# Optimization experiments

Hardware: AMD Instinct MI355X
Metric: run time of the kernel (lower is better)

The kernel has to match this reference:

```python
import jax, jax.numpy as jnp
import numpy as np

B, N, D, E = 4, 8192, 8, 128
SCALE = float(1.0 / np.sqrt(E))  # torch MHA scaling, n_heads=1 -> head_dim=E


def _attn_dir(X, idx, mask, Wq, Wk, Wv, ipw, ipb, ow, ob):
    # X: [B,N,E]; idx, mask: [B,N,D]. Sequence per node = [self] + padded neighbors.
    neigh = jax.vmap(lambda x, i: x[i])(X, idx)               # [B,N,D,E] gather
    seq = jnp.concatenate([X[:, :, None, :], neigh], axis=2)  # [B,N,1+D,E]
    m = jnp.concatenate([jnp.ones(mask.shape[:2] + (1,), bool), mask.astype(bool)], axis=2)
    wq, wk, wv = jnp.split(ipw, 3, axis=0)                    # torch in_proj_weight [3E,E]
    bq, bk, bv = jnp.split(ipb, 3)
    # custom pre-projections (X @ W), then torch MHA in_proj (x @ w.T + b)
    q = (X @ Wq) @ wq.T + bq                                  # [B,N,E]; only self row queried
    k = (seq @ Wk) @ wk.T + bk                                # [B,N,1+D,E]
    v = (seq @ Wv) @ wv.T + bv                                # [B,N,1+D,E]
    scores = jnp.einsum('bne,bnse->bns', q, k) * SCALE
    scores = jnp.where(m, scores, jnp.finfo(scores.dtype).min)
    w = jax.nn.softmax(scores, axis=-1)
    ctx = jnp.einsum('bns,bnse->bne', w, v)
    return ctx @ ow.T + ob                                    # MHA out_proj


def setup_inputs():
    key = jax.random.key(0)
    ks = jax.random.split(key, 26)
    f32 = jnp.float32
    inp = {
        "X": jax.random.normal(ks[0], (B, N, E), f32),
        "in_idx": jax.random.randint(ks[1], (B, N, D), 0, N, dtype=jnp.int32),
        "out_idx": jax.random.randint(ks[2], (B, N, D), 0, N, dtype=jnp.int32),
        "in_mask": jax.random.randint(ks[3], (B, N, D), 0, 2, dtype=jnp.int32),
        "out_mask": jax.random.randint(ks[4], (B, N, D), 0, 2, dtype=jnp.int32),
    }
    i = 5
    for pfx in ("in_", "out_"):
        inp[pfx + "Wq"] = jax.random.uniform(ks[i], (E, E), f32) * 0.1; i += 1
        inp[pfx + "Wk"] = jax.random.uniform(ks[i], (E, E), f32) * 0.1; i += 1
        inp[pfx + "Wv"] = jax.random.uniform(ks[i], (E, E), f32) * 0.1; i += 1
        inp[pfx + "ipw"] = jax.random.normal(ks[i], (3 * E, E), f32) * 0.05; i += 1
        inp[pfx + "ipb"] = jax.random.normal(ks[i], (3 * E,), f32) * 0.02; i += 1
        inp[pfx + "ow"] = jax.random.normal(ks[i], (E, E), f32) * 0.05; i += 1
        inp[pfx + "ob"] = jax.random.normal(ks[i], (E,), f32) * 0.02; i += 1
    inp["lin_w"] = jax.random.normal(ks[i], (E, 2 * E), f32) * 0.05; i += 1
    inp["lin_b"] = jax.random.normal(ks[i], (E,), f32) * 0.02
    return inp


def reference(X, in_idx, out_idx, in_mask, out_mask,
              in_Wq, in_Wk, in_Wv, in_ipw, in_ipb, in_ow, in_ob,
              out_Wq, out_Wk, out_Wv, out_ipw, out_ipb, out_ow, out_ob,
              lin_w, lin_b):
    a_in = _attn_dir(X, in_idx, in_mask, in_Wq, in_Wk, in_Wv, in_ipw, in_ipb, in_ow, in_ob)
    a_out = _attn_dir(X, out_idx, out_mask, out_Wq, out_Wk, out_Wv, out_ipw, out_ipb, out_ow, out_ob)
    h = jnp.concatenate([a_in, a_out], axis=-1) @ lin_w.T + lin_b  # [B,N,E]
    return jax.nn.elu(h)
```

## Files before the change

### kernel.cpp

```cpp
#include <hip/hip_runtime.h>
#include <math.h>

#define NNODE 32768
constexpr float SCALE = 0.08838834764831845f;

typedef unsigned short u16;
typedef __bf16 bf16x8 __attribute__((ext_vector_type(8)));
typedef float f32x4 __attribute__((ext_vector_type(4)));

__device__ __forceinline__ u16 f2bf(float f) {
    unsigned u = __float_as_uint(f);
    u += 0x7fff + ((u >> 16) & 1);
    return (u16)(u >> 16);
}
__device__ __forceinline__ unsigned pack2bf(float lo, float hi) {
    return (unsigned)f2bf(lo) | ((unsigned)f2bf(hi) << 16);
}
__device__ __forceinline__ void unpack8(uint4 u, float* f) {
    f[0] = __uint_as_float(u.x << 16);  f[1] = __uint_as_float(u.x & 0xffff0000u);
    f[2] = __uint_as_float(u.y << 16);  f[3] = __uint_as_float(u.y & 0xffff0000u);
    f[4] = __uint_as_float(u.z << 16);  f[5] = __uint_as_float(u.z & 0xffff0000u);
    f[6] = __uint_as_float(u.w << 16);  f[7] = __uint_as_float(u.w & 0xffff0000u);
}
__device__ __forceinline__ float dot128(const float* __restrict__ a,
                                        const float* __restrict__ b) {
    float s = 0.f;
    #pragma unroll
    for (int c = 0; c < 128; c += 4) {
        float4 x = *(const float4*)&a[c];
        float4 y = *(const float4*)&b[c];
        s = fmaf(x.x, y.x, s); s = fmaf(x.y, y.y, s);
        s = fmaf(x.z, y.z, s); s = fmaf(x.w, y.w, s);
    }
    return s;
}

__device__ __forceinline__ void gl_lds16(const void* g, void* l) {
    __builtin_amdgcn_global_load_lds(
        (const __attribute__((address_space(1))) unsigned int*)(uintptr_t)g,
        (__attribute__((address_space(3))) unsigned int*)(unsigned int)(uintptr_t)l,
        16, 0, 0);
}

__global__ __launch_bounds__(256) void wprep1(
    const float* __restrict__ ipw_in, const float* __restrict__ ipw_out,
    const float* __restrict__ Wq_in, const float* __restrict__ Wk_in,
    const float* __restrict__ Wv_in,
    const float* __restrict__ Wq_out, const float* __restrict__ Wk_out,
    const float* __restrict__ Wv_out,
    const float* __restrict__ ow_in, const float* __restrict__ ow_out,
    const float* __restrict__ lin_w,
    float* __restrict__ Af, float* __restrict__ Bmf,
    float* __restrict__ Wtf, float* __restrict__ RTf)
{
    int t = blockIdx.x * 256 + threadIdx.x;
    int i = t >> 7, j = t & 127;
    int task = blockIdx.y, dir = task & 1, kind = task >> 1;
    if (kind < 3) {
        const float* ipw = dir ? ipw_out : ipw_in;
        const float* W; const float* w; float* outp;
        if (kind == 0)      { W = dir ? Wq_out : Wq_in; w = ipw;          outp = Af;  }
        else if (kind == 1) { W = dir ? Wk_out : Wk_in; w = ipw + 16384;  outp = Bmf; }
        else                { W = dir ? Wv_out : Wv_in; w = ipw + 32768;  outp = Wtf; }
        outp[dir * 16384 + i * 128 + j] = dot128(W + i * 128, w + j * 128);
    } else {
        const float* ow = dir ? ow_out : ow_in;
        const float* lw = lin_w + i * 256 + dir * 128;
        float s = 0.f;
        #pragma unroll
        for (int e = 0; e < 128; e += 4) {
            float4 l4 = *(const float4*)&lw[e];
            s = fmaf(ow[e * 128 + j],       l4.x, s);
            s = fmaf(ow[(e + 1) * 128 + j], l4.y, s);
            s = fmaf(ow[(e + 2) * 128 + j], l4.z, s);
            s = fmaf(ow[(e + 3) * 128 + j], l4.w, s);
        }
        RTf[dir * 16384 + i * 128 + j] = s;
    }
}

__global__ __launch_bounds__(256) void wprep2(
    const float* __restrict__ Af, const float* __restrict__ Bmf,
    const float* __restrict__ Wtf, const float* __restrict__ RTf,
    const float* __restrict__ ipb_in, const float* __restrict__ ipb_out,
    const float* __restrict__ lin_w, const float* __restrict__ lin_b,
    const float* __restrict__ ob_in, const float* __restrict__ ob_out,
    u16* __restrict__ Bcat, u16* __restrict__ QfT,
    float* __restrict__ ycat, float* __restrict__ bfin)
{
    int task = blockIdx.y;
    int t = blockIdx.x * 256 + threadIdx.x;
    if (task < 2) {
        int dir = task, i = t >> 7, j = t & 127;
        float s = dot128(Af + dir * 16384 + j * 128, Bmf + dir * 16384 + i * 128);
        Bcat[(size_t)(dir * 128 + i) * 128 + j] = f2bf(s);
    } else if (task < 4) {
        int dir = task - 2, i = t >> 7, j = t & 127;
        float s = dot128(Wtf + dir * 16384 + j * 128, RTf + dir * 16384 + i * 128);
        QfT[(size_t)i * 256 + dir * 128 + j] = f2bf(s);
    } else {
        if (t < 256) {
            int dir = t >> 7, d = t & 127;
            const float* bq = dir ? ipb_out : ipb_in;
            const float* rb = Bmf + dir * 16384 + d * 128;
            float s = 0.f;
            for (int f = 0; f < 128; ++f) s = fmaf(rb[f], bq[f], s);
            ycat[t] = s;
        } else if (t < 384) {
            int g = t - 256;
            float s = lin_b[g];
            #pragma unroll
            for (int dir = 0; dir < 2; ++dir) {
                const float* bv = (dir ? ipb_out : ipb_in) + 256;
                const float* rt = RTf + dir * 16384 + g * 128;
                const float* ob = dir ? ob_out : ob_in;
                const float* lw = lin_w + g * 256 + dir * 128;
                for (int c = 0; c < 128; ++c)
                    s += bv[c] * rt[c] + ob[c] * lw[c];
            }
            bfin[g] = s;
        }
    }
}

template<int NT>
__global__ __launch_bounds__(256) void gemm_y(
    const float* __restrict__ X,
    const u16* __restrict__ BT,
    const float* __restrict__ bias,
    u16* __restrict__ C, u16* __restrict__ Xb)
{
    __shared__ __align__(16) u16 As[128 * 128];
    __shared__ __align__(16) u16 Bs[128 * 128];
    const int tid  = threadIdx.x;
    const int lane = tid & 63;
    const int wid  = tid >> 6;
    const int bm  = blockIdx.x * 128;
    const int wr = wid >> 1, wc = wid & 1;
    const int l15 = lane & 15, l4 = lane >> 4;

    #pragma unroll
    for (int i = 0; i < 8; ++i) {
        int c = i * 256 + tid;
        int r = c >> 4, cb = c & 15;
        const float* src = &X[(size_t)(bm + r) * 128 + cb * 8];
        float4 f0 = *(const float4*)src;
        float4 f1 = *(const float4*)(src + 4);
        uint4 pk;
        pk.x = pack2bf(f0.x, f0.y); pk.y = pack2bf(f0.z, f0.w);
        pk.z = pack2bf(f1.x, f1.y); pk.w = pack2bf(f1.z, f1.w);
        *(uint4*)&As[r * 128 + ((cb ^ (r & 7)) * 8)] = pk;
        *(uint4*)&Xb[(size_t)(bm + r) * 128 + cb * 8] = pk;
    }
    __syncthreads();
    bf16x8 a[4][4];
    #pragma unroll
    for (int ks = 0; ks < 4; ++ks)
        #pragma unroll
        for (int mr = 0; mr < 4; ++mr) {
            int r = wr * 64 + mr * 16 + l15;
            int kb = ks * 4 + l4;
            a[ks][mr] = *(const bf16x8*)((const char*)As + r * 256 + ((kb ^ (r & 7)) << 4));
        }

    #pragma unroll
    for (int nt = 0; nt < NT; ++nt) {
        int bn = nt * 128;
        __syncthreads();
        #pragma unroll
        for (int i = 0; i < 8; ++i) {
            int c = i * 256 + tid;
            int r = c >> 4, cb = c & 15;
            gl_lds16(&BT[(size_t)(bn + r) * 128 + 8 * (cb ^ (r & 7))],
                     &Bs[(size_t)(c - lane) * 8]);
        }
        __syncthreads();

        f32x4 acc[4][4] = {};
        #pragma unroll
        for (int ks = 0; ks < 4; ++ks) {
            bf16x8 bfr[4];
            #pragma unroll
            for (int nc = 0; nc < 4; ++nc) {
                int r = wc * 64 + nc * 16 + l15;
                int kb = ks * 4 + l4;
                bfr[nc] = *(const bf16x8*)((const char*)Bs + r * 256 + ((kb ^ (r & 7)) << 4));
            }
            #pragma unroll
            for (int mr = 0; mr < 4; ++mr)
                #pragma unroll
                for (int nc = 0; nc < 4; ++nc)
                    acc[mr][nc] = __builtin_amdgcn_mfma_f32_16x16x32_bf16(
                        a[ks][mr], bfr[nc], acc[mr][nc], 0, 0, 0);
        }
        #pragma unroll
        for (int nc = 0; nc < 4; ++nc) {
            int col = bn + wc * 64 + nc * 16 + l15;
            float bv = bias[col];
            #pragma unroll
            for (int mr = 0; mr < 4; ++mr)
                #pragma unroll
                for (int j = 0; j < 4; ++j) {
                    int row = bm + wr * 64 + mr * 16 + l4 * 4 + j;
                    C[(size_t)row * 256 + col] = f2bf(acc[mr][nc][j] + bv);
                }
        }
    }
}

template<int KTOT, bool ELU_F32>
__global__ __launch_bounds__(256) void gemm_mfma(
    const u16* __restrict__ A,
    const u16* __restrict__ BT,
    const float* __restrict__ bias,
    void* __restrict__ Cout, int ldc)
{
    __shared__ __align__(16) u16 As[128 * 128];
    __shared__ __align__(16) u16 Bs[128 * 128];
    const int tid  = threadIdx.x;
    const int lane = tid & 63;
    const int wid  = tid >> 6;
    const int bm = blockIdx.x * 128;
    const int bn = blockIdx.y * 128;
    const int wr = wid >> 1, wc = wid & 1;
    const int l15 = lane & 15, l4 = lane >> 4;

    f32x4 acc[4][4] = {};

    for (int k0 = 0; k0 < KTOT; k0 += 128) {
        #pragma unroll
        for (int i = 0; i < 8; ++i) {
            int c = i * 256 + tid;
            int r = c >> 4, cb = c & 15;
            int col = k0 + 8 * (cb ^ (r & 7));
            gl_lds16(&A[(size_t)(bm + r) * KTOT + col], &As[(size_t)(c - lane) * 8]);
            gl_lds16(&BT[(size_t)(bn + r) * KTOT + col], &Bs[(size_t)(c - lane) * 8]);
        }
        __syncthreads();
        #pragma unroll
        for (int ks = 0; ks < 4; ++ks) {
            bf16x8 a[4], b[4];
            #pragma unroll
            for (int mr = 0; mr < 4; ++mr) {
                int r = wr * 64 + mr * 16 + l15;
                int kb = ks * 4 + l4;
                a[mr] = *(const bf16x8*)((const char*)As + r * 256 + ((kb ^ (r & 7)) << 4));
            }
            #pragma unroll
            for (int nc = 0; nc < 4; ++nc) {
                int r = wc * 64 + nc * 16 + l15;
                int kb = ks * 4 + l4;
                b[nc] = *(const bf16x8*)((const char*)Bs + r * 256 + ((kb ^ (r & 7)) << 4));
            }
            #pragma unroll
            for (int mr = 0; mr < 4; ++mr)
                #pragma unroll
                for (int nc = 0; nc < 4; ++nc)
                    acc[mr][nc] = __builtin_amdgcn_mfma_f32_16x16x32_bf16(
                        a[mr], b[nc], acc[mr][nc], 0, 0, 0);
        }
        __syncthreads();
    }

    #pragma unroll
    for (int nc = 0; nc < 4; ++nc) {
        int col = bn + wc * 64 + nc * 16 + l15;
        float bv = bias[col];
        #pragma unroll
        for (int mr = 0; mr < 4; ++mr) {
            #pragma unroll
            for (int j = 0; j < 4; ++j) {
                int row = bm + wr * 64 + mr * 16 + l4 * 4 + j;
                float v = acc[mr][nc][j] + bv;
                if (ELU_F32) {
                    v = v > 0.f ? v : (__expf(v) - 1.f);
                    ((float*)Cout)[(size_t)row * ldc + col] = v;
                } else {
                    ((u16*)Cout)[(size_t)row * ldc + col] = f2bf(v);
                }
            }
        }
    }
}

__global__ __launch_bounds__(256) void attn_kernel(
    const u16* __restrict__ Y, const u16* __restrict__ Xb,
    const int* __restrict__ in_idx, const int* __restrict__ out_idx,
    const int* __restrict__ in_mask, const int* __restrict__ out_mask,
    u16* __restrict__ XCTX)
{
    const int tid = threadIdx.x;
    const int g   = tid >> 4;
    const int l   = tid & 15;
    const int pair = blockIdx.x & 7;
    const int dir = pair & 1, b = pair >> 1;
    const int nl = ((blockIdx.x >> 3) << 4) + g;
    const int node = (b << 13) + nl;
    const int* idx = dir == 0 ? in_idx : out_idx;
    const int* msk = dir == 0 ? in_mask : out_mask;

    const int4 i0 = *(const int4*)&idx[(size_t)node * 8];
    const int4 i1 = *(const int4*)&idx[(size_t)node * 8 + 4];
    const int4 m0 = *(const int4*)&msk[(size_t)node * 8];
    const int4 m1 = *(const int4*)&msk[(size_t)node * 8 + 4];
    const int ii[8] = { i0.x, i0.y, i0.z, i0.w, i1.x, i1.y, i1.z, i1.w };
    const int mm[8] = { m0.x, m0.y, m0.z, m0.w, m1.x, m1.y, m1.z, m1.w };

    uint4 yv = *(const uint4*)&Y[(size_t)node * 256 + dir * 128 + l * 8];
    uint4 xv[9];
    xv[0] = *(const uint4*)&Xb[(size_t)node * 128 + l * 8];
    #pragma unroll
    for (int s = 0; s < 8; ++s)
        xv[s + 1] = *(const uint4*)&Xb[(size_t)((b << 13) + ii[s]) * 128 + l * 8];

    float yf[8];
    unpack8(yv, yf);
    float sc[9];
    #pragma unroll
    for (int s = 0; s < 9; ++s) {
        float kf[8];
        unpack8(xv[s], kf);
        float d = 0.f;
        #pragma unroll
        for (int j = 0; j < 8; ++j) d = fmaf(yf[j], kf[j], d);
        sc[s] = d;
    }

    #pragma unroll
    for (int s = 0; s < 9; ++s) {
        float x = sc[s];
        x += __shfl_xor(x, 1);
        x += __shfl_xor(x, 2);
        x += __shfl_xor(x, 4);
        x += __shfl_xor(x, 8);
        sc[s] = x * SCALE;
    }
    #pragma unroll
    for (int s = 1; s < 9; ++s)
        sc[s] = mm[s - 1] ? sc[s] : -1e30f;

    float m = sc[0];
    #pragma unroll
    for (int s = 1; s < 9; ++s) m = fmaxf(m, sc[s]);
    float w[9], wsum = 0.f;
    #pragma unroll
    for (int s = 0; s < 9; ++s) { w[s] = __expf(sc[s] - m); wsum += w[s]; }
    const float inv = 1.f / wsum;

    float acc[8] = {};
    #pragma unroll
    for (int s = 0; s < 9; ++s) {
        float vf[8];
        unpack8(xv[s], vf);
        #pragma unroll
        for (int j = 0; j < 8; ++j) acc[j] = fmaf(w[s], vf[j], acc[j]);
    }
    uint4 o;
    o.x = pack2bf(acc[0] * inv, acc[1] * inv);
    o.y = pack2bf(acc[2] * inv, acc[3] * inv);
    o.z = pack2bf(acc[4] * inv, acc[5] * inv);
    o.w = pack2bf(acc[6] * inv, acc[7] * inv);
    *(uint4*)&XCTX[(size_t)node * 256 + dir * 128 + l * 8] = o;
}

extern "C" void kernel_launch(void* const* d_in, const int* in_sizes, int n_in,
                              void* d_out, int out_size, void* d_ws, size_t ws_size,
                              hipStream_t stream) {
    const float* X        = (const float*)d_in[0];
    const int*   in_idx   = (const int*)d_in[1];
    const int*   out_idx  = (const int*)d_in[2];
    const int*   in_mask  = (const int*)d_in[3];
    const int*   out_mask = (const int*)d_in[4];
    const float* Wq_in  = (const float*)d_in[5];
    const float* Wk_in  = (const float*)d_in[6];
    const float* Wv_in  = (const float*)d_in[7];
    const float* ipw_in = (const float*)d_in[8];
    const float* ipb_in = (const float*)d_in[9];
    const float* ow_in  = (const float*)d_in[10];
    const float* ob_in  = (const float*)d_in[11];
    const float* Wq_out  = (const float*)d_in[12];
    const float* Wk_out  = (const float*)d_in[13];
    const float* Wv_out  = (const float*)d_in[14];
    const float* ipw_out = (const float*)d_in[15];
    const float* ipb_out = (const float*)d_in[16];
    const float* ow_out  = (const float*)d_in[17];
    const float* ob_out  = (const float*)d_in[18];
    const float* lin_w   = (const float*)d_in[19];
    const float* lin_b   = (const float*)d_in[20];

    char* wsb = (char*)d_ws;
    u16*   Xbw  = (u16*)(wsb + 0);
    u16*   Yw   = (u16*)(wsb + 8388608);
    u16*   XCTX = (u16*)(wsb + 25165824);
    u16*   Bcat = (u16*)(wsb + 41943040);
    u16*   QfT  = (u16*)(wsb + 42008576);
    float* Af   = (float*)(wsb + 42074112);
    float* Bmf  = (float*)(wsb + 42205184);
    float* Wtf  = (float*)(wsb + 42336256);
    float* RTf  = (float*)(wsb + 42467328);
    float* ycat = (float*)(wsb + 42598400);
    float* bfin = (float*)(wsb + 42599424);

    wprep1<<<dim3(64, 8), 256, 0, stream>>>(
        ipw_in, ipw_out, Wq_in, Wk_in, Wv_in, Wq_out, Wk_out, Wv_out,
        ow_in, ow_out, lin_w, Af, Bmf, Wtf, RTf);

    wprep2<<<dim3(64, 5), 256, 0, stream>>>(
        Af, Bmf, Wtf, RTf, ipb_in, ipb_out, lin_w, lin_b, ob_in, ob_out,
        Bcat, QfT, ycat, bfin);

    gemm_y<2><<<dim3(256, 1), 256, 0, stream>>>(X, Bcat, ycat, Yw, Xbw);

    attn_kernel<<<4096, 256, 0, stream>>>(
        Yw, Xbw, in_idx, out_idx, in_mask, out_mask, XCTX);

    gemm_mfma<256, true><<<dim3(256, 1), 256, 0, stream>>>(
        XCTX, QfT, bfin, (float*)d_out, 128);
}
```

Baseline: 69.06 us.

## Fuse Y-projection GEMM, attention and output GEMM into one kernel

Moves the X-to-bf16 conversion into the weight-prep kernel, then replaces the three-kernel chain (Y GEMM, gather attention, final GEMM with ELU) with a single kernel that handles 32 nodes per block. Y and the attention context stay in LDS instead of round-tripping through global memory, and two launches are removed. In exchange, the GEMM tiles are much smaller and B operands are read straight from global memory without LDS staging, so MFMA efficiency drops. Neighbor gathers of Xb still go to global memory.

```diff
diff --git a/kernel.cpp b/kernel.cpp
--- a/kernel.cpp
+++ b/kernel.cpp
@@ -42,7 +42,8 @@
         16, 0, 0);
 }
 
-__global__ __launch_bounds__(256) void wprep1(
+__global__ __launch_bounds__(256) void prep(
+    const float* __restrict__ X, u16* __restrict__ Xb,
     const float* __restrict__ ipw_in, const float* __restrict__ ipw_out,
     const float* __restrict__ Wq_in, const float* __restrict__ Wk_in,
     const float* __restrict__ Wv_in,
@@ -53,9 +54,21 @@
     float* __restrict__ Af, float* __restrict__ Bmf,
     float* __restrict__ Wtf, float* __restrict__ RTf)
 {
-    int t = blockIdx.x * 256 + threadIdx.x;
+    if (blockIdx.x < 2048) {
+        int t = blockIdx.x * 256 + threadIdx.x;
+        float4 a = *(const float4*)&X[(size_t)t * 8];
+        float4 b = *(const float4*)&X[(size_t)t * 8 + 4];
+        uint4 pk;
+        pk.x = pack2bf(a.x, a.y); pk.y = pack2bf(a.z, a.w);
+        pk.z = pack2bf(b.x, b.y); pk.w = pack2bf(b.z, b.w);
+        *(uint4*)&Xb[(size_t)t * 8] = pk;
+        return;
+    }
+    int flat = blockIdx.x - 2048;
+    int task = flat >> 6, blk = flat & 63;
+    int t = blk * 256 + threadIdx.x;
     int i = t >> 7, j = t & 127;
-    int task = blockIdx.y, dir = task & 1, kind = task >> 1;
+    int dir = task & 1, kind = task >> 1;
     if (kind < 3) {
         const float* ipw = dir ? ipw_out : ipw_in;
         const float* W; const float* w; float* outp;
@@ -123,244 +136,194 @@
     }
 }
 
-template<int NT>
-__global__ __launch_bounds__(256) void gemm_y(
-    const float* __restrict__ X,
-    const u16* __restrict__ BT,
-    const float* __restrict__ bias,
-    u16* __restrict__ C, u16* __restrict__ Xb)
+__global__ __launch_bounds__(256) void mega(
+    const u16* __restrict__ Xb, const u16* __restrict__ Bcat,
+    const float* __restrict__ ycat, const u16* __restrict__ QfT,
+    const float* __restrict__ bfin,
+    const int* __restrict__ in_idx, const int* __restrict__ out_idx,
+    const int* __restrict__ in_mask, const int* __restrict__ out_mask,
+    float* __restrict__ Cout)
 {
-    __shared__ __align__(16) u16 As[128 * 128];
-    __shared__ __align__(16) u16 Bs[128 * 128];
+    __shared__ __align__(16) u16 XbT[32 * 128];
+    __shared__ __align__(16) u16 Yl[32 * 256];
+    __shared__ __align__(16) u16 XC[32 * 256];
+
     const int tid  = threadIdx.x;
     const int lane = tid & 63;
     const int wid  = tid >> 6;
-    const int bm  = blockIdx.x * 128;
-    const int wr = wid >> 1, wc = wid & 1;
-    const int l15 = lane & 15, l4 = lane >> 4;
+    const int l15  = lane & 15, l4 = lane >> 4;
+
+    const int bid  = blockIdx.x;
+    const int b    = (bid & 7) >> 1;
+    const int s    = ((bid >> 3) << 1) + (bid & 1);
+    const int node0 = (b << 13) + s * 32;
 
     #pragma unroll
-    for (int i = 0; i < 8; ++i) {
+    for (int i = 0; i < 2; ++i) {
         int c = i * 256 + tid;
         int r = c >> 4, cb = c & 15;
-        const float* src = &X[(size_t)(bm + r) * 128 + cb * 8];
-        float4 f0 = *(const float4*)src;
-        float4 f1 = *(const float4*)(src + 4);
-        uint4 pk;
-        pk.x = pack2bf(f0.x, f0.y); pk.y = pack2bf(f0.z, f0.w);
-        pk.z = pack2bf(f1.x, f1.y); pk.w = pack2bf(f1.z, f1.w);
-        *(uint4*)&As[r * 128 + ((cb ^ (r & 7)) * 8)] = pk;
-        *(uint4*)&Xb[(size_t)(bm + r) * 128 + cb * 8] = pk;
+        gl_lds16(&Xb[(size_t)(node0 + r) * 128 + 8 * (cb ^ (r & 7))],
+                 &XbT[(size_t)(c - lane) * 8]);
     }
     __syncthreads();
-    bf16x8 a[4][4];
-    #pragma unroll
-    for (int ks = 0; ks < 4; ++ks)
-        #pragma unroll
-        for (int mr = 0; mr < 4; ++mr) {
-            int r = wr * 64 + mr * 16 + l15;
-            int kb = ks * 4 + l4;
-            a[ks][mr] = *(const bf16x8*)((const char*)As + r * 256 + ((kb ^ (r & 7)) << 4));
-        }
-
-    #pragma unroll
-    for (int nt = 0; nt < NT; ++nt) {
-        int bn = nt * 128;
-        __syncthreads();
-        #pragma unroll
-        for (int i = 0; i < 8; ++i) {
-            int c = i * 256 + tid;
-            int r = c >> 4, cb = c & 15;
-            gl_lds16(&BT[(size_t)(bn + r) * 128 + 8 * (cb ^ (r & 7))],
-                     &Bs[(size_t)(c - lane) * 8]);
-        }
-        __syncthreads();
-
-        f32x4 acc[4][4] = {};
+
+    {
+        f32x4 acc[2][4] = {};
         #pragma unroll
         for (int ks = 0; ks < 4; ++ks) {
-            bf16x8 bfr[4];
+            bf16x8 a[2], bb[4];
+            #pragma unroll
+            for (int mr = 0; mr < 2; ++mr) {
+                int r = mr * 16 + l15;
+                int kb = ks * 4 + l4;
+                a[mr] = *(const bf16x8*)((const char*)XbT + r * 256 + ((kb ^ (r & 7)) << 4));
+            }
             #pragma unroll
             for (int nc = 0; nc < 4; ++nc) {
-                int r = wc * 64 + nc * 16 + l15;
-                int kb = ks * 4 + l4;
-                bfr[nc] = *(const bf16x8*)((const char*)Bs + r * 256 + ((kb ^ (r & 7)) << 4));
-            }
-            #pragma unroll
-            for (int mr = 0; mr < 4; ++mr)
+                int col = wid * 64 + nc * 16 + l15;
+                bb[nc] = *(const bf16x8*)&Bcat[(size_t)col * 128 + (ks * 4 + l4) * 8];
+            }
+            #pragma unroll
+            for (int mr = 0; mr < 2; ++mr)
                 #pragma unroll
                 for (int nc = 0; nc < 4; ++nc)
                     acc[mr][nc] = __builtin_amdgcn_mfma_f32_16x16x32_bf16(
-                        a[ks][mr], bfr[nc], acc[mr][nc], 0, 0, 0);
-        }
-        #pragma unroll
-        for (int nc = 0; nc < 4; ++nc) {
-            int col = bn + wc * 64 + nc * 16 + l15;
-            float bv = bias[col];
-            #pragma unroll
-            for (int mr = 0; mr < 4; ++mr)
+                        a[mr], bb[nc], acc[mr][nc], 0, 0, 0);
+        }
+        float yb[4];
+        #pragma unroll
+        for (int nc = 0; nc < 4; ++nc) yb[nc] = ycat[wid * 64 + nc * 16 + l15];
+        #pragma unroll
+        for (int mr = 0; mr < 2; ++mr)
+            #pragma unroll
+            for (int nc = 0; nc < 4; ++nc) {
+                int col = wid * 64 + nc * 16 + l15;
+                int chunk = col >> 3, within = col & 7;
                 #pragma unroll
                 for (int j = 0; j < 4; ++j) {
-                    int row = bm + wr * 64 + mr * 16 + l4 * 4 + j;
-                    C[(size_t)row * 256 + col] = f2bf(acc[mr][nc][j] + bv);
+                    int row = mr * 16 + l4 * 4 + j;
+                    *(u16*)((char*)Yl + row * 512 + ((chunk ^ (row & 7)) << 4) + within * 2)
+                        = f2bf(acc[mr][nc][j] + yb[nc]);
                 }
-        }
-    }
-}
-
-template<int KTOT, bool ELU_F32>
-__global__ __launch_bounds__(256) void gemm_mfma(
-    const u16* __restrict__ A,
-    const u16* __restrict__ BT,
-    const float* __restrict__ bias,
-    void* __restrict__ Cout, int ldc)
-{
-    __shared__ __align__(16) u16 As[128 * 128];
-    __shared__ __align__(16) u16 Bs[128 * 128];
-    const int tid  = threadIdx.x;
-    const int lane = tid & 63;
-    const int wid  = tid >> 6;
-    const int bm = blockIdx.x * 128;
-    const int bn = blockIdx.y * 128;
-    const int wr = wid >> 1, wc = wid & 1;
-    const int l15 = lane & 15, l4 = lane >> 4;
-
-    f32x4 acc[4][4] = {};
-
-    for (int k0 = 0; k0 < KTOT; k0 += 128) {
-        #pragma unroll
-        for (int i = 0; i < 8; ++i) {
-            int c = i * 256 + tid;
-            int r = c >> 4, cb = c & 15;
-            int col = k0 + 8 * (cb ^ (r & 7));
-            gl_lds16(&A[(size_t)(bm + r) * KTOT + col], &As[(size_t)(c - lane) * 8]);
-            gl_lds16(&BT[(size_t)(bn + r) * KTOT + col], &Bs[(size_t)(c - lane) * 8]);
-        }
-        __syncthreads();
-        #pragma unroll
-        for (int ks = 0; ks < 4; ++ks) {
-            bf16x8 a[4], b[4];
-            #pragma unroll
-            for (int mr = 0; mr < 4; ++mr) {
-                int r = wr * 64 + mr * 16 + l15;
+            }
+    }
+    __syncthreads();
+
+    {
+        const int g = tid >> 4, l = tid & 15;
+        #pragma unroll
+        for (int round = 0; round < 4; ++round) {
+            int item = round * 16 + g;
+            int r   = item & 31;
+            int dir = item >> 5;
+            int node = node0 + r;
+            const int* idx = dir ? out_idx : in_idx;
+            const int* msk = dir ? out_mask : in_mask;
+
+            const int4 i0 = *(const int4*)&idx[(size_t)node * 8];
+            const int4 i1 = *(const int4*)&idx[(size_t)node * 8 + 4];
+            const int4 m0 = *(const int4*)&msk[(size_t)node * 8];
+            const int4 m1 = *(const int4*)&msk[(size_t)node * 8 + 4];
+            const int ii[8] = { i0.x, i0.y, i0.z, i0.w, i1.x, i1.y, i1.z, i1.w };
+            const int mm[8] = { m0.x, m0.y, m0.z, m0.w, m1.x, m1.y, m1.z, m1.w };
+
+            uint4 yv = *(const uint4*)((const char*)Yl + r * 512 +
+                           ((((dir << 4) + l) ^ (r & 7)) << 4));
+            uint4 xv[9];
+            xv[0] = *(const uint4*)((const char*)XbT + r * 256 + ((l ^ (r & 7)) << 4));
+            #pragma unroll
+            for (int t2 = 0; t2 < 8; ++t2)
+                xv[t2 + 1] = *(const uint4*)&Xb[(size_t)((b << 13) + ii[t2]) * 128 + l * 8];
+
+            float yf[8];
+            unpack8(yv, yf);
+            float sc[9];
+            #pragma unroll
+            for (int t2 = 0; t2 < 9; ++t2) {
+                float kf[8];
+                unpack8(xv[t2], kf);
+                float d = 0.f;
+                #pragma unroll
+                for (int j = 0; j < 8; ++j) d = fmaf(yf[j], kf[j], d);
+                sc[t2] = d;
+            }
+            #pragma unroll
+            for (int t2 = 0; t2 < 9; ++t2) {
+                float x = sc[t2];
+                x += __shfl_xor(x, 1);
+                x += __shfl_xor(x, 2);
+                x += __shfl_xor(x, 4);
+                x += __shfl_xor(x, 8);
+                sc[t2] = x * SCALE;
+            }
+            #pragma unroll
+            for (int t2 = 1; t2 < 9; ++t2)
+                sc[t2] = mm[t2 - 1] ? sc[t2] : -1e30f;
+
+            float m = sc[0];
+            #pragma unroll
+            for (int t2 = 1; t2 < 9; ++t2) m = fmaxf(m, sc[t2]);
+            float w[9], wsum = 0.f;
+            #pragma unroll
+            for (int t2 = 0; t2 < 9; ++t2) { w[t2] = __expf(sc[t2] - m); wsum += w[t2]; }
+            const float inv = 1.f / wsum;
+
+            float acc[8] = {};
+            #pragma unroll
+            for (int t2 = 0; t2 < 9; ++t2) {
+                float vf[8];
+                unpack8(xv[t2], vf);
+                #pragma unroll
+                for (int j = 0; j < 8; ++j) acc[j] = fmaf(w[t2], vf[j], acc[j]);
+            }
+            uint4 o;
+            o.x = pack2bf(acc[0] * inv, acc[1] * inv);
+            o.y = pack2bf(acc[2] * inv, acc[3] * inv);
+            o.z = pack2bf(acc[4] * inv, acc[5] * inv);
+            o.w = pack2bf(acc[6] * inv, acc[7] * inv);
+            *(uint4*)((char*)XC + r * 512 + ((((dir << 4) + l) ^ (r & 7)) << 4)) = o;
+        }
+    }
+    __syncthreads();
+
+    {
+        f32x4 acc[2][2] = {};
+        #pragma unroll
+        for (int ks = 0; ks < 8; ++ks) {
+            bf16x8 a[2], bb[2];
+            #pragma unroll
+            for (int mr = 0; mr < 2; ++mr) {
+                int r = mr * 16 + l15;
                 int kb = ks * 4 + l4;
-                a[mr] = *(const bf16x8*)((const char*)As + r * 256 + ((kb ^ (r & 7)) << 4));
-            }
-            #pragma unroll
-            for (int nc = 0; nc < 4; ++nc) {
-                int r = wc * 64 + nc * 16 + l15;
-                int kb = ks * 4 + l4;
-                b[nc] = *(const bf16x8*)((const char*)Bs + r * 256 + ((kb ^ (r & 7)) << 4));
-            }
-            #pragma unroll
-            for (int mr = 0; mr < 4; ++mr)
-                #pragma unroll
-                for (int nc = 0; nc < 4; ++nc)
+                a[mr] = *(const bf16x8*)((const char*)XC + r * 512 + ((kb ^ (r & 7)) << 4));
+            }
+            #pragma unroll
+            for (int nc = 0; nc < 2; ++nc) {
+                int col = wid * 32 + nc * 16 + l15;
+                bb[nc] = *(const bf16x8*)&QfT[(size_t)col * 256 + (ks * 4 + l4) * 8];
+            }
+            #pragma unroll
+            for (int mr = 0; mr < 2; ++mr)
+                #pragma unroll
+                for (int nc = 0; nc < 2; ++nc)
                     acc[mr][nc] = __builtin_amdgcn_mfma_f32_16x16x32_bf16(
-                        a[mr], b[nc], acc[mr][nc], 0, 0, 0);
-        }
-        __syncthreads();
-    }
-
-    #pragma unroll
-    for (int nc = 0; nc < 4; ++nc) {
-        int col = bn + wc * 64 + nc * 16 + l15;
-        float bv = bias[col];
-        #pragma unroll
-        for (int mr = 0; mr < 4; ++mr) {
-            #pragma unroll
-            for (int j = 0; j < 4; ++j) {
-                int row = bm + wr * 64 + mr * 16 + l4 * 4 + j;
-                float v = acc[mr][nc][j] + bv;
-                if (ELU_F32) {
+                        a[mr], bb[nc], acc[mr][nc], 0, 0, 0);
+        }
+        #pragma unroll
+        for (int nc = 0; nc < 2; ++nc) {
+            int col = wid * 32 + nc * 16 + l15;
+            float bv = bfin[col];
+            #pragma unroll
+            for (int mr = 0; mr < 2; ++mr)
+                #pragma unroll
+                for (int j = 0; j < 4; ++j) {
+                    int row = mr * 16 + l4 * 4 + j;
+                    float v = acc[mr][nc][j] + bv;
                     v = v > 0.f ? v : (__expf(v) - 1.f);
-                    ((float*)Cout)[(size_t)row * ldc + col] = v;
-                } else {
-                    ((u16*)Cout)[(size_t)row * ldc + col] = f2bf(v);
+                    Cout[(size_t)(node0 + row) * 128 + col] = v;
                 }
-            }
-        }
-    }
-}
-
-__global__ __launch_bounds__(256) void attn_kernel(
-    const u16* __restrict__ Y, const u16* __restrict__ Xb,
-    const int* __restrict__ in_idx, const int* __restrict__ out_idx,
-    const int* __restrict__ in_mask, const int* __restrict__ out_mask,
-    u16* __restrict__ XCTX)
-{
-    const int tid = threadIdx.x;
-    const int g   = tid >> 4;
-    const int l   = tid & 15;
-    const int pair = blockIdx.x & 7;
-    const int dir = pair & 1, b = pair >> 1;
-    const int nl = ((blockIdx.x >> 3) << 4) + g;
-    const int node = (b << 13) + nl;
-    const int* idx = dir == 0 ? in_idx : out_idx;
-    const int* msk = dir == 0 ? in_mask : out_mask;
-
-    const int4 i0 = *(const int4*)&idx[(size_t)node * 8];
-    const int4 i1 = *(const int4*)&idx[(size_t)node * 8 + 4];
-    const int4 m0 = *(const int4*)&msk[(size_t)node * 8];
-    const int4 m1 = *(const int4*)&msk[(size_t)node * 8 + 4];
-    const int ii[8] = { i0.x, i0.y, i0.z, i0.w, i1.x, i1.y, i1.z, i1.w };
-    const int mm[8] = { m0.x, m0.y, m0.z, m0.w, m1.x, m1.y, m1.z, m1.w };
-
-    uint4 yv = *(const uint4*)&Y[(size_t)node * 256 + dir * 128 + l * 8];
-    uint4 xv[9];
-    xv[0] = *(const uint4*)&Xb[(size_t)node * 128 + l * 8];
-    #pragma unroll
-    for (int s = 0; s < 8; ++s)
-        xv[s + 1] = *(const uint4*)&Xb[(size_t)((b << 13) + ii[s]) * 128 + l * 8];
-
-    float yf[8];
-    unpack8(yv, yf);
-    float sc[9];
-    #pragma unroll
-    for (int s = 0; s < 9; ++s) {
-        float kf[8];
-        unpack8(xv[s], kf);
-        float d = 0.f;
-        #pragma unroll
-        for (int j = 0; j < 8; ++j) d = fmaf(yf[j], kf[j], d);
-        sc[s] = d;
-    }
-
-    #pragma unroll
-    for (int s = 0; s < 9; ++s) {
-        float x = sc[s];
-        x += __shfl_xor(x, 1);
-        x += __shfl_xor(x, 2);
-        x += __shfl_xor(x, 4);
-        x += __shfl_xor(x, 8);
-        sc[s] = x * SCALE;
-    }
-    #pragma unroll
-    for (int s = 1; s < 9; ++s)
-        sc[s] = mm[s - 1] ? sc[s] : -1e30f;
-
-    float m = sc[0];
-    #pragma unroll
-    for (int s = 1; s < 9; ++s) m = fmaxf(m, sc[s]);
-    float w[9], wsum = 0.f;
-    #pragma unroll
-    for (int s = 0; s < 9; ++s) { w[s] = __expf(sc[s] - m); wsum += w[s]; }
-    const float inv = 1.f / wsum;
-
-    float acc[8] = {};
-    #pragma unroll
-    for (int s = 0; s < 9; ++s) {
-        float vf[8];
-        unpack8(xv[s], vf);
-        #pragma unroll
-        for (int j = 0; j < 8; ++j) acc[j] = fmaf(w[s], vf[j], acc[j]);
-    }
-    uint4 o;
-    o.x = pack2bf(acc[0] * inv, acc[1] * inv);
-    o.y = pack2bf(acc[2] * inv, acc[3] * inv);
-    o.z = pack2bf(acc[4] * inv, acc[5] * inv);
-    o.w = pack2bf(acc[6] * inv, acc[7] * inv);
-    *(uint4*)&XCTX[(size_t)node * 256 + dir * 128 + l * 8] = o;
+        }
+    }
 }
 
 extern "C" void kernel_launch(void* const* d_in, const int* in_sizes, int n_in,
@@ -390,30 +353,24 @@
 
     char* wsb = (char*)d_ws;
     u16*   Xbw  = (u16*)(wsb + 0);
-    u16*   Yw   = (u16*)(wsb + 8388608);
-    u16*   XCTX = (u16*)(wsb + 25165824);
-    u16*   Bcat = (u16*)(wsb + 41943040);
-    u16*   QfT  = (u16*)(wsb + 42008576);
-    float* Af   = (float*)(wsb + 42074112);
-    float* Bmf  = (float*)(wsb + 42205184);
-    float* Wtf  = (float*)(wsb + 42336256);
-    float* RTf  = (float*)(wsb + 42467328);
-    float* ycat = (float*)(wsb + 42598400);
-    float* bfin = (float*)(wsb + 42599424);
-
-    wprep1<<<dim3(64, 8), 256, 0, stream>>>(
-        ipw_in, ipw_out, Wq_in, Wk_in, Wv_in, Wq_out, Wk_out, Wv_out,
+    u16*   Bcat = (u16*)(wsb + 8388608);
+    u16*   QfT  = (u16*)(wsb + 8454144);
+    float* Af   = (float*)(wsb + 8519680);
+    float* Bmf  = (float*)(wsb + 8650752);
+    float* Wtf  = (float*)(wsb + 8781824);
+    float* RTf  = (float*)(wsb + 8912896);
+    float* ycat = (float*)(wsb + 9043968);
+    float* bfin = (float*)(wsb + 9044992);
+
+    prep<<<2560, 256, 0, stream>>>(
+        X, Xbw, ipw_in, ipw_out, Wq_in, Wk_in, Wv_in, Wq_out, Wk_out, Wv_out,
         ow_in, ow_out, lin_w, Af, Bmf, Wtf, RTf);
 
     wprep2<<<dim3(64, 5), 256, 0, stream>>>(
         Af, Bmf, Wtf, RTf, ipb_in, ipb_out, lin_w, lin_b, ob_in, ob_out,
         Bcat, QfT, ycat, bfin);
 
-    gemm_y<2><<<dim3(256, 1), 256, 0, stream>>>(X, Bcat, ycat, Yw, Xbw);
-
-    attn_kernel<<<4096, 256, 0, stream>>>(
-        Yw, Xbw, in_idx, out_idx, in_mask, out_mask, XCTX);
-
-    gemm_mfma<256, true><<<dim3(256, 1), 256, 0, stream>>>(
-        XCTX, QfT, bfin, (float*)d_out, 128);
-}
+    mega<<<1024, 256, 0, stream>>>(
+        Xbw, Bcat, ycat, QfT, bfin,
+        in_idx, out_idx, in_mask, out_mask, (float*)d_out);
+}
```

New measurement: 84.56 us. 22.4% more time.
